# Performance work log

Measured on AMD Instinct MI355X. Metric: run time of the kernel, lower is better.

## Reference

```python
import jax, jax.numpy as jnp
import numpy as np

# Correlation layer constants (match init_kwargs / torch defaults)
MAX_DISP = 20      # max_displacement
STRIDE2 = 2
KERNEL = 3         # kernel_size (only used in the normalization)
D = 2 * MAX_DISP + 1  # 41 displacement steps per axis


def setup_inputs() -> dict:
    key = jax.random.key(0)
    k1, k2 = jax.random.split(key)
    b, c, h, w = 4, 64, 96, 160
    input1 = jax.random.normal(k1, (b, c, h, w), dtype=jnp.float32)
    input2 = jax.random.normal(k2, (b, c, h, w), dtype=jnp.float32)
    return {"input1": input1, "input2": input2}


def _correlation(input1, input2):
    b, c, h, w = input1.shape
    # displacement offsets: (i - max_displacement//2) * stride2, i in [0, D)
    offs = (jnp.arange(D) - MAX_DISP // 2) * STRIDE2  # ranges -20 .. +60
    # output channel m = i*D + j uses dx = offs[i] (W shift), dy = offs[j] (H shift)
    dxs = jnp.repeat(offs, D)  # [D*D]
    dys = jnp.tile(offs, D)    # [D*D]
    P = int((D - 1 - MAX_DISP // 2) * STRIDE2)  # = 60, max |shift|
    padded = jnp.pad(input2, ((0, 0), (0, 0), (P, P), (P, P)))
    # shifted[..., y, x] = input2[..., y - dy, x - dx] (zero outside)
    def step(carry, disp):
        dy, dx = disp
        sl = jax.lax.dynamic_slice(padded, (0, 0, P - dy, P - dx), (b, c, h, w))
        return carry, (input1 * sl).sum(axis=1)  # [b, h, w]
    _, out = jax.lax.scan(step, None, (dys, dxs))  # [D*D, b, h, w]
    out = jnp.transpose(out, (1, 0, 2, 3))  # [b, D*D, h, w]
    return out / (c * KERNEL * KERNEL)


def reference(input1, input2):
    return _correlation(input1, input2)
```

## Files before the change

### kernel.cpp

```cpp
#include <hip/hip_runtime.h>
#include <hip/hip_bf16.h>


#define B_ 4
#define C_ 64
#define H_ 96
#define W_ 160
#define DD 41
#define HW_ (H_*W_)
#define RS 72
#define GS 161

typedef __bf16 bf16x8 __attribute__((ext_vector_type(8)));
typedef float  f32x4  __attribute__((ext_vector_type(4)));

__global__ void to_nhwc(const float* __restrict__ s1, const float* __restrict__ s2,
                        ushort* __restrict__ d1, ushort* __restrict__ d2) {
    int p = blockIdx.x * 256 + threadIdx.x;
    const float* src = blockIdx.y ? s2 : s1;
    ushort* dst = blockIdx.y ? d2 : d1;
    int b = p / HW_;
    int rem = p - b * HW_;
    const float* sp = src + (size_t)b * (C_ * HW_) + rem;
    ushort tmp[C_];
#pragma unroll
    for (int c = 0; c < C_; ++c) {
        union { float f; unsigned u; } uu;
        uu.f = sp[(size_t)c * HW_];
        unsigned r = uu.u + 0x7FFF + ((uu.u >> 16) & 1);
        tmp[c] = (ushort)(r >> 16);
    }
    uint4* dp = (uint4*)(dst + (size_t)p * C_);
#pragma unroll
    for (int k = 0; k < 8; ++k) dp[k] = ((uint4*)tmp)[k];
}

__global__ __launch_bounds__(256) void corr_kernel(const ushort* __restrict__ in1w,
                                                   const ushort* __restrict__ in2w,
                                                   float* __restrict__ out) {
    __shared__ ushort s2[2 * 80 * RS];
    __shared__ float  gd[DD * GS];

    const int j   = blockIdx.x;
    const int y   = blockIdx.y;
    const int b   = blockIdx.z;
    const int tid = threadIdx.x;
    const int lane = tid & 63;
    const int w    = tid >> 6;
    const int y2 = y + 20 - 2 * j;
    const bool valid_row = (y2 >= 0) && (y2 < H_);

    if (valid_row) {
        const uint4* src = (const uint4*)(in2w + (size_t)((b * H_ + y2) * W_) * C_);
#pragma unroll
        for (int it = 0; it < 5; ++it) {
            int cidx = it * 256 + tid;
            int u  = cidx >> 3;
            int co = (cidx & 7) * 8;
            uint4 v = src[cidx];
            *(uint4*)&s2[((u & 1) * 80 + (u >> 1)) * RS + co] = v;
        }
        __syncthreads();

        const int quad = lane >> 4;
        const int l15  = lane & 15;
        const ushort* a_base = in1w + (size_t)((b * H_ + y) * W_) * C_;
        for (int t = 0; t < 10; ++t) {
            int p  = w * 10 + t;
            int mi = p >> 2;
            int nt = p & 3;
            int par = (mi >= 5) ? 1 : 0;
            int x0  = (mi - 5 * par) * 32;
            int xa = x0 + par + 2 * l15;
            const bf16x8* aptr = (const bf16x8*)(const void*)(a_base + xa * C_ + quad * 8);
            bf16x8 a0 = aptr[0];
            bf16x8 a1 = aptr[4];
            int u0 = x0 + par - 60 + 32 * nt;
            int u  = u0 + 2 * l15;
            bf16x8 b0 = {}, b1 = {};
            if (u >= 0 && u < W_) {
                const bf16x8* bptr =
                    (const bf16x8*)(const void*)&s2[((u & 1) * 80 + (u >> 1)) * RS + quad * 8];
                b0 = bptr[0];
                b1 = bptr[4];
            }
            f32x4 acc = {};
            acc = __builtin_amdgcn_mfma_f32_16x16x32_bf16(a0, b0, acc, 0, 0, 0);
            acc = __builtin_amdgcn_mfma_f32_16x16x32_bf16(a1, b1, acc, 0, 0, 0);
#pragma unroll
            for (int r = 0; r < 4; ++r) {
                int mx = quad * 4 + r;
                int i  = mx - l15 - 16 * nt + 40;
                if (i >= 0 && i <= 40) {
                    int x = x0 + par + 2 * mx;
                    gd[i * GS + x] = acc[r];
                }
            }
        }
        __syncthreads();
    }

    const float scale = 1.0f / 576.0f;
    for (int i = w; i < DD; i += 4) {
        float* op = out + ((size_t)(b * (DD * DD) + i * DD + j) * H_ + y) * W_;
        if (valid_row) {
            op[lane]       = gd[i * GS + lane] * scale;
            op[lane + 64]  = gd[i * GS + lane + 64] * scale;
            if (lane < 32) op[lane + 128] = gd[i * GS + lane + 128] * scale;
        } else {
            op[lane]      = 0.0f;
            op[lane + 64] = 0.0f;
            if (lane < 32) op[lane + 128] = 0.0f;
        }
    }
}

extern "C" void kernel_launch(void* const* d_in, const int* in_sizes, int n_in,
                              void* d_out, int out_size, void* d_ws, size_t ws_size,
                              hipStream_t stream) {
    const float* in1 = (const float*)d_in[0];
    const float* in2 = (const float*)d_in[1];
    float* out = (float*)d_out;
    ushort* w1 = (ushort*)d_ws;
    ushort* w2 = w1 + (size_t)B_ * H_ * W_ * C_;
    to_nhwc<<<dim3((B_ * HW_) / 256, 2), 256, 0, stream>>>(in1, in2, w1, w2);
    corr_kernel<<<dim3(DD, H_, B_), 256, 0, stream>>>(w1, w2, out);
}
```

Before: 535.0 us.

## Drop LDS staging of input2 row, reorder grid, use nontemporal loads/stores

The correlation kernel no longer stages the input2 row into shared memory. Each warp now owns one n-tile and reads B fragments straight from global memory, which removes a barrier and reduces LDS use so more blocks can be resident (launch bounds now request 4 per SM). The grid is reordered so that blocks sharing the same displacement row j and neighbouring (b,y) run adjacently, and the large output is written with nontemporal stores to avoid polluting the cache. The conversion kernel's input reads are also made nontemporal. The cost is redundant global/L2 reads of input2 across warps instead of one shared copy.

```diff
diff --git a/kernel.cpp b/kernel.cpp
--- a/kernel.cpp
+++ b/kernel.cpp
@@ -8,7 +8,6 @@
 #define W_ 160
 #define DD 41
 #define HW_ (H_*W_)
-#define RS 72
 #define GS 161
 
 typedef __bf16 bf16x8 __attribute__((ext_vector_type(8)));
@@ -26,7 +25,7 @@
 #pragma unroll
     for (int c = 0; c < C_; ++c) {
         union { float f; unsigned u; } uu;
-        uu.f = sp[(size_t)c * HW_];
+        uu.f = __builtin_nontemporal_load(&sp[(size_t)c * HW_]);
         unsigned r = uu.u + 0x7FFF + ((uu.u >> 16) & 1);
         tmp[c] = (ushort)(r >> 16);
     }
@@ -35,52 +34,37 @@
     for (int k = 0; k < 8; ++k) dp[k] = ((uint4*)tmp)[k];
 }
 
-__global__ __launch_bounds__(256) void corr_kernel(const ushort* __restrict__ in1w,
-                                                   const ushort* __restrict__ in2w,
-                                                   float* __restrict__ out) {
-    __shared__ ushort s2[2 * 80 * RS];
-    __shared__ float  gd[DD * GS];
+__global__ __launch_bounds__(256, 4) void corr_kernel(const ushort* __restrict__ in1w,
+                                                      const ushort* __restrict__ in2w,
+                                                      float* __restrict__ out) {
+    __shared__ float gd[DD * GS];
 
-    const int j   = blockIdx.x;
-    const int y   = blockIdx.y;
-    const int b   = blockIdx.z;
-    const int tid = threadIdx.x;
-    const int lane = tid & 63;
-    const int w    = tid >> 6;
+    const int bx = blockIdx.x;
+    const int j  = blockIdx.y;
+    const int b  = bx / H_;
+    const int y  = bx - b * H_;
+    const int lane = threadIdx.x & 63;
+    const int w    = threadIdx.x >> 6;
+    const int quad = lane >> 4;
+    const int l15  = lane & 15;
     const int y2 = y + 20 - 2 * j;
     const bool valid_row = (y2 >= 0) && (y2 < H_);
 
     if (valid_row) {
-        const uint4* src = (const uint4*)(in2w + (size_t)((b * H_ + y2) * W_) * C_);
-#pragma unroll
-        for (int it = 0; it < 5; ++it) {
-            int cidx = it * 256 + tid;
-            int u  = cidx >> 3;
-            int co = (cidx & 7) * 8;
-            uint4 v = src[cidx];
-            *(uint4*)&s2[((u & 1) * 80 + (u >> 1)) * RS + co] = v;
-        }
-        __syncthreads();
-
-        const int quad = lane >> 4;
-        const int l15  = lane & 15;
         const ushort* a_base = in1w + (size_t)((b * H_ + y) * W_) * C_;
-        for (int t = 0; t < 10; ++t) {
-            int p  = w * 10 + t;
-            int mi = p >> 2;
-            int nt = p & 3;
-            int par = (mi >= 5) ? 1 : 0;
-            int x0  = (mi - 5 * par) * 32;
-            int xa = x0 + par + 2 * l15;
+        const ushort* b_base = in2w + (size_t)((b * H_ + y2) * W_) * C_;
+#pragma unroll 2
+        for (int mi = 0; mi < 10; ++mi) {
+            const int par = (mi >= 5) ? 1 : 0;
+            const int x0  = (mi - 5 * par) * 32;
+            const int xa = x0 + par + 2 * l15;
             const bf16x8* aptr = (const bf16x8*)(const void*)(a_base + xa * C_ + quad * 8);
             bf16x8 a0 = aptr[0];
             bf16x8 a1 = aptr[4];
-            int u0 = x0 + par - 60 + 32 * nt;
-            int u  = u0 + 2 * l15;
+            const int u = x0 + par - 60 + 32 * w + 2 * l15;
             bf16x8 b0 = {}, b1 = {};
             if (u >= 0 && u < W_) {
-                const bf16x8* bptr =
-                    (const bf16x8*)(const void*)&s2[((u & 1) * 80 + (u >> 1)) * RS + quad * 8];
+                const bf16x8* bptr = (const bf16x8*)(const void*)(b_base + u * C_ + quad * 8);
                 b0 = bptr[0];
                 b1 = bptr[4];
             }
@@ -89,11 +73,10 @@
             acc = __builtin_amdgcn_mfma_f32_16x16x32_bf16(a1, b1, acc, 0, 0, 0);
 #pragma unroll
             for (int r = 0; r < 4; ++r) {
-                int mx = quad * 4 + r;
-                int i  = mx - l15 - 16 * nt + 40;
+                const int mx = quad * 4 + r;
+                const int i  = mx - l15 - 16 * w + 40;
                 if (i >= 0 && i <= 40) {
-                    int x = x0 + par + 2 * mx;
-                    gd[i * GS + x] = acc[r];
+                    gd[i * GS + x0 + par + 2 * mx] = acc[r];
                 }
             }
         }
@@ -104,13 +87,15 @@
     for (int i = w; i < DD; i += 4) {
         float* op = out + ((size_t)(b * (DD * DD) + i * DD + j) * H_ + y) * W_;
         if (valid_row) {
-            op[lane]       = gd[i * GS + lane] * scale;
-            op[lane + 64]  = gd[i * GS + lane + 64] * scale;
-            if (lane < 32) op[lane + 128] = gd[i * GS + lane + 128] * scale;
+            __builtin_nontemporal_store(gd[i * GS + lane] * scale, &op[lane]);
+            __builtin_nontemporal_store(gd[i * GS + lane + 64] * scale, &op[lane + 64]);
+            if (lane < 32)
+                __builtin_nontemporal_store(gd[i * GS + lane + 128] * scale, &op[lane + 128]);
         } else {
-            op[lane]      = 0.0f;
-            op[lane + 64] = 0.0f;
-            if (lane < 32) op[lane + 128] = 0.0f;
+            __builtin_nontemporal_store(0.0f, &op[lane]);
+            __builtin_nontemporal_store(0.0f, &op[lane + 64]);
+            if (lane < 32)
+                __builtin_nontemporal_store(0.0f, &op[lane + 128]);
         }
     }
 }
@@ -124,5 +109,5 @@
     ushort* w1 = (ushort*)d_ws;
     ushort* w2 = w1 + (size_t)B_ * H_ * W_ * C_;
     to_nhwc<<<dim3((B_ * HW_) / 256, 2), 256, 0, stream>>>(in1, in2, w1, w2);
-    corr_kernel<<<dim3(DD, H_, B_), 256, 0, stream>>>(w1, w2, out);
+    corr_kernel<<<dim3(B_ * H_, DD), 256, 0, stream>>>(w1, w2, out);
 }
```

Result: slower. 580.5 us (+8.5%).
